# Optimization experiments

Hardware: AMD Instinct MI355X
Metric: run time of the kernel (lower is better)

## Reference

```python
import jax, jax.numpy as jnp
import numpy as np

N, E, F_IN, HID, HEADS, OUT, G = 50000, 800000, 128, 64, 4, 10, 64
NEG_SLOPE = 0.2


def _glorot(key, shape):
    fan = shape[0] + shape[-1]
    lim = np.sqrt(6.0 / fan)
    return jax.random.uniform(key, shape, jnp.float32, -lim, lim)


def setup_inputs() -> dict:
    key = jax.random.key(0)
    ks = jax.random.split(key, 20)
    x = jax.random.normal(ks[0], (N, F_IN), jnp.float32)
    edge_index = jax.random.randint(ks[1], (2, E), 0, N, jnp.int64)
    batch = jnp.sort(jax.random.randint(ks[2], (N,), 0, G, jnp.int64))
    inp = {"x": x, "edge_index": edge_index, "batch": batch}
    # layer 1: in=F_IN, heads=HEADS, out=HID
    inp["W1"] = _glorot(ks[3], (F_IN, HEADS * HID))
    inp["b1"] = jnp.zeros((HEADS * HID,), jnp.float32)
    inp["as1"] = _glorot(ks[4], (HEADS, HID))
    inp["ad1"] = _glorot(ks[5], (HEADS, HID))
    # layer 2: in=HEADS*HID, heads=HEADS, out=HID
    inp["W2"] = _glorot(ks[6], (HEADS * HID, HEADS * HID))
    inp["b2"] = jnp.zeros((HEADS * HID,), jnp.float32)
    inp["as2"] = _glorot(ks[7], (HEADS, HID))
    inp["ad2"] = _glorot(ks[8], (HEADS, HID))
    # layer 3: in=HEADS*HID, heads=1, out=HID
    inp["W3"] = _glorot(ks[9], (HEADS * HID, HID))
    inp["b3"] = jnp.zeros((HID,), jnp.float32)
    inp["as3"] = _glorot(ks[10], (1, HID))
    inp["ad3"] = _glorot(ks[11], (1, HID))
    # MLP head [HID, HID, OUT]
    inp["Wm1"] = _glorot(ks[12], (HID, HID))
    inp["bm1"] = jnp.zeros((HID,), jnp.float32)
    inp["Wm2"] = _glorot(ks[13], (HID, OUT))
    inp["bm2"] = jnp.zeros((OUT,), jnp.float32)
    return inp


def _gat_layer(x, src, dst, W, b, att_src, att_dst):
    # x: [N, Fin]; att_*: [H, C]
    H, C = att_src.shape
    h = (x @ W).reshape(N, H, C)
    a_src = jnp.einsum("nhc,hc->nh", h, att_src)
    a_dst = jnp.einsum("nhc,hc->nh", h, att_dst)
    alpha = jax.nn.leaky_relu(a_src[src] + a_dst[dst], NEG_SLOPE)  # [E', H]
    amax = jax.ops.segment_max(alpha, dst, num_segments=N)
    alpha = jnp.exp(alpha - amax[dst])
    denom = jax.ops.segment_sum(alpha, dst, num_segments=N)
    alpha = alpha / (denom[dst] + 1e-16)
    msg = h[src] * alpha[:, :, None]  # [E', H, C]
    out = jax.ops.segment_sum(msg, dst, num_segments=N)  # [N, H, C]
    return out.reshape(N, H * C) + b


def reference(x, edge_index, batch, W1, b1, as1, ad1, W2, b2, as2, ad2, W3, b3, as3, ad3, Wm1, bm1, Wm2, bm2):
    # PyG GATConv adds self-loops by default
    loops = jnp.arange(N, dtype=edge_index.dtype)
    src = jnp.concatenate([edge_index[0], loops])
    dst = jnp.concatenate([edge_index[1], loops])
    h = jax.nn.relu(_gat_layer(x, src, dst, W1, b1, as1, ad1))
    h = jax.nn.relu(_gat_layer(h, src, dst, W2, b2, as2, ad2))
    h = jax.nn.relu(_gat_layer(h, src, dst, W3, b3, as3, ad3))
    pooled = jax.ops.segment_sum(h, batch, num_segments=G)  # [G, HID]
    hidden = jax.nn.relu(pooled @ Wm1 + bm1)
    return hidden @ Wm2 + bm2
```

## Files before the change

kernel.cpp:

```cpp
#include <hip/hip_runtime.h>
#include <hip/hip_bf16.h>

#define F_IN   128
#define HID    64
#define HEADS  4
#define OUTD   10
#define NGRP   64

typedef unsigned short u16;
typedef __attribute__((ext_vector_type(8))) short short8;
typedef __attribute__((ext_vector_type(4))) float f32x4;

__device__ __forceinline__ float atomAddF(float* p, float v) {
    return __hip_atomic_fetch_add(p, v, __ATOMIC_RELAXED, __HIP_MEMORY_SCOPE_AGENT);
}
__device__ __forceinline__ float lrelu(float f) { return f > 0.f ? f : 0.2f * f; }
__device__ __forceinline__ float b2f(u16 u) { return __uint_as_float(((unsigned)u) << 16); }
__device__ __forceinline__ u16 f2b(float f) {
    unsigned u = __float_as_uint(f);
    return (u16)((u + 0x7fffu + ((u >> 16) & 1u)) >> 16);
}
__device__ __forceinline__ unsigned fmono(float f) {
    unsigned u = __float_as_uint(f);
    return (u & 0x80000000u) ? ~u : (u | 0x80000000u);
}
__device__ __forceinline__ float funmono(unsigned u) {
    return __uint_as_float((u & 0x80000000u) ? (u & 0x7FFFFFFFu) : ~u);
}

__global__ __launch_bounds__(256) void wtrans_all_kernel(const float* __restrict__ W1,
                                                         const float* __restrict__ W2,
                                                         const float* __restrict__ W3,
                                                         u16* __restrict__ Wt1,
                                                         u16* __restrict__ Wt2,
                                                         u16* __restrict__ Wt3) {
    int i = blockIdx.x * 256 + threadIdx.x;
    if (i < 32768) {
        int n = i >> 7, k = i & 127;
        Wt1[i] = f2b(W1[(size_t)k * 256 + n]);
    } else if (i < 98304) {
        int j = i - 32768;
        int n = j >> 8, k = j & 255;
        Wt2[j] = f2b(W2[(size_t)k * 256 + n]);
    } else if (i < 114688) {
        int j = i - 98304;
        int n = j >> 8, k = j & 255;
        Wt3[j] = f2b(W3[(size_t)k * 64 + n]);
    }
}

template<int K, int NC, bool AF32>
__global__ __launch_bounds__(256) void gemm_att_kernel(const void* __restrict__ Aptr,
                                                       const u16* __restrict__ Bt,
                                                       const float* __restrict__ as_,
                                                       const float* __restrict__ ad_,
                                                       u16* __restrict__ Hb,
                                                       float* __restrict__ a_src,
                                                       float* __restrict__ a_dst,
                                                       unsigned* __restrict__ gmaxu,
                                                       int nrows) {
    constexpr int LDA = 40;
    constexpr int HH = NC / 64;
    __shared__ u16 As[64][LDA];
    __shared__ u16 Bs[NC][LDA];
    int tid = threadIdx.x;
    int m0 = blockIdx.x * 64;
    int w = tid >> 6, l = tid & 63, lr = l & 15, lk = l >> 4;

    if constexpr (NC == 256) {
        f32x4 acc[4][4] = {};
        for (int k0 = 0; k0 < K; k0 += 32) {
            {
                int row = tid >> 2, ks = (tid & 3) * 8;
                int grow = m0 + row;
                short8 av = {};
                if (grow < nrows) {
                    if constexpr (AF32) {
                        const float* src = (const float*)Aptr + (size_t)grow * K + k0 + ks;
                        float4 v0 = *(const float4*)src;
                        float4 v1 = *(const float4*)(src + 4);
                        av[0] = (short)f2b(v0.x); av[1] = (short)f2b(v0.y);
                        av[2] = (short)f2b(v0.z); av[3] = (short)f2b(v0.w);
                        av[4] = (short)f2b(v1.x); av[5] = (short)f2b(v1.y);
                        av[6] = (short)f2b(v1.z); av[7] = (short)f2b(v1.w);
                    } else {
                        av = *(const short8*)&((const u16*)Aptr)[(size_t)grow * K + k0 + ks];
                    }
                }
                *(short8*)&As[row][ks] = av;
            }
            #pragma unroll
            for (int i = 0; i < 4; i++) {
                int col = (tid >> 2) + 64 * i;
                int ks = (tid & 3) * 8;
                *(short8*)&Bs[col][ks] = *(const short8*)&Bt[(size_t)col * K + k0 + ks];
            }
            __syncthreads();
            short8 a[4], b[4];
            #pragma unroll
            for (int mi = 0; mi < 4; mi++) a[mi] = *(const short8*)&As[16 * mi + lr][lk * 8];
            #pragma unroll
            for (int ni = 0; ni < 4; ni++) b[ni] = *(const short8*)&Bs[64 * w + 16 * ni + lr][lk * 8];
            #pragma unroll
            for (int mi = 0; mi < 4; mi++)
                #pragma unroll
                for (int ni = 0; ni < 4; ni++)
                    acc[mi][ni] = __builtin_amdgcn_mfma_f32_16x16x32_bf16(a[mi], b[ni], acc[mi][ni], 0, 0, 0);
            __syncthreads();
        }
        #pragma unroll
        for (int mi = 0; mi < 4; mi++) {
            #pragma unroll
            for (int j = 0; j < 4; j++) {
                int grow = m0 + 16 * mi + lk * 4 + j;
                if (grow < nrows) {
                    #pragma unroll
                    for (int ni = 0; ni < 4; ni++)
                        Hb[(size_t)grow * NC + 64 * w + 16 * ni + lr] = f2b(acc[mi][ni][j]);
                }
            }
        }
        float asv[4], adv[4];
        #pragma unroll
        for (int ni = 0; ni < 4; ni++) {
            asv[ni] = as_[w * 64 + 16 * ni + lr];
            adv[ni] = ad_[w * 64 + 16 * ni + lr];
        }
        float mxs = -3.4e38f;
        #pragma unroll
        for (int mi = 0; mi < 4; mi++) {
            #pragma unroll
            for (int j = 0; j < 4; j++) {
                float ps = 0.f, pd = 0.f;
                #pragma unroll
                for (int ni = 0; ni < 4; ni++) {
                    float v = acc[mi][ni][j];
                    ps += v * asv[ni];
                    pd += v * adv[ni];
                }
                #pragma unroll
                for (int o = 1; o < 16; o <<= 1) {
                    ps += __shfl_xor(ps, o, 64);
                    pd += __shfl_xor(pd, o, 64);
                }
                mxs = fmaxf(mxs, ps);
                int grow = m0 + 16 * mi + lk * 4 + j;
                if (lr == 0 && grow < nrows) {
                    a_src[grow * HH + w] = ps;
                    a_dst[grow * HH + w] = pd;
                }
            }
        }
        mxs = fmaxf(mxs, __shfl_xor(mxs, 16, 64));
        mxs = fmaxf(mxs, __shfl_xor(mxs, 32, 64));
        if (l == 0) atomicMax(&gmaxu[w], fmono(mxs));
    } else {
        f32x4 acc[4] = {};
        for (int k0 = 0; k0 < K; k0 += 32) {
            {
                int row = tid >> 2, ks = (tid & 3) * 8;
                int grow = m0 + row;
                short8 av = {};
                if (grow < nrows) av = *(const short8*)&((const u16*)Aptr)[(size_t)grow * K + k0 + ks];
                *(short8*)&As[row][ks] = av;
            }
            {
                int col = tid >> 2;
                int ks = (tid & 3) * 8;
                *(short8*)&Bs[col][ks] = *(const short8*)&Bt[(size_t)col * K + k0 + ks];
            }
            __syncthreads();
            short8 af = *(const short8*)&As[16 * w + lr][lk * 8];
            #pragma unroll
            for (int c = 0; c < 4; c++) {
                short8 bf = *(const short8*)&Bs[c * 16 + lr][lk * 8];
                acc[c] = __builtin_amdgcn_mfma_f32_16x16x32_bf16(af, bf, acc[c], 0, 0, 0);
            }
            __syncthreads();
        }
        #pragma unroll
        for (int c = 0; c < 4; c++) {
            #pragma unroll
            for (int j = 0; j < 4; j++) {
                int grow = m0 + 16 * w + lk * 4 + j;
                if (grow < nrows) Hb[(size_t)grow * NC + c * 16 + lr] = f2b(acc[c][j]);
            }
        }
        float asv[4], adv[4];
        #pragma unroll
        for (int c = 0; c < 4; c++) {
            asv[c] = as_[c * 16 + lr];
            adv[c] = ad_[c * 16 + lr];
        }
        float mxs = -3.4e38f;
        #pragma unroll
        for (int j = 0; j < 4; j++) {
            float ps = 0.f, pd = 0.f;
            #pragma unroll
            for (int c = 0; c < 4; c++) {
                float v = acc[c][j];
                ps += v * asv[c];
                pd += v * adv[c];
            }
            #pragma unroll
            for (int o = 1; o < 16; o <<= 1) {
                ps += __shfl_xor(ps, o, 64);
                pd += __shfl_xor(pd, o, 64);
            }
            mxs = fmaxf(mxs, ps);
            int grow = m0 + 16 * w + lk * 4 + j;
            if (lr == 0 && grow < nrows) {
                a_src[grow] = ps;
                a_dst[grow] = pd;
            }
        }
        mxs = fmaxf(mxs, __shfl_xor(mxs, 16, 64));
        mxs = fmaxf(mxs, __shfl_xor(mxs, 32, 64));
        if (l == 0) atomicMax(&gmaxu[0], fmono(mxs));
    }
}

__global__ void count_kernel(const int* __restrict__ ei, int* __restrict__ deg,
                             int E_, int n_nodes) {
    int e = blockIdx.x * 256 + threadIdx.x;
    int tot = E_ + n_nodes;
    if (e >= tot) return;
    int d = (e < E_) ? ei[E_ + e] : e - E_;
    atomicAdd(&deg[d], 1);
}

__global__ __launch_bounds__(256) void scan_reduce_kernel(const int* __restrict__ deg,
                                                          int* __restrict__ bsum, int n) {
    int i = blockIdx.x * 256 + threadIdx.x;
    int v = (i < n) ? deg[i] : 0;
    #pragma unroll
    for (int o = 32; o; o >>= 1) v += __shfl_xor(v, o, 64);
    __shared__ int ws[4];
    if ((threadIdx.x & 63) == 0) ws[threadIdx.x >> 6] = v;
    __syncthreads();
    if (threadIdx.x == 0) bsum[blockIdx.x] = ws[0] + ws[1] + ws[2] + ws[3];
}

__global__ __launch_bounds__(256) void scan_blocksums_kernel(int* __restrict__ bsum, int nb) {
    __shared__ int s[256];
    int t = threadIdx.x;
    int v = (t < nb) ? bsum[t] : 0;
    s[t] = v;
    __syncthreads();
    #pragma unroll
    for (int d = 1; d < 256; d <<= 1) {
        int x = (t >= d) ? s[t - d] : 0;
        __syncthreads();
        s[t] += x;
        __syncthreads();
    }
    if (t < nb) bsum[t] = s[t] - v;
}

__global__ __launch_bounds__(256) void scan_final_kernel(const int* __restrict__ deg,
                                                         const int* __restrict__ bsum,
                                                         int* __restrict__ off, int n) {
    __shared__ int s[256];
    int t = threadIdx.x;
    int i = blockIdx.x * 256 + t;
    int v = (i < n) ? deg[i] : 0;
    s[t] = v;
    __syncthreads();
    #pragma unroll
    for (int d = 1; d < 256; d <<= 1) {
        int x = (t >= d) ? s[t - d] : 0;
        __syncthreads();
        s[t] += x;
        __syncthreads();
    }
    int ex = s[t] - v + bsum[blockIdx.x];
    if (i < n) off[i] = ex;
    if (i == n - 1) off[n] = ex + v;
}

__global__ void fill_kernel(const int* __restrict__ ei, const int* __restrict__ off,
                            int* __restrict__ cursor, int* __restrict__ csr_src,
                            int E_, int n_nodes) {
    int e = blockIdx.x * 256 + threadIdx.x;
    int tot = E_ + n_nodes;
    if (e >= tot) return;
    int s, d;
    if (e < E_) { s = ei[e]; d = ei[E_ + e]; } else { s = d = e - E_; }
    int pos = atomicAdd(&cursor[d], 1);
    csr_src[off[d] + pos] = s;
}

template<int HH, int CPL, bool OUTF32>
__global__ __launch_bounds__(256) void gat_aggr_kernel(const int* __restrict__ off,
                                                       const int* __restrict__ csr_src,
                                                       const u16* __restrict__ Hb,
                                                       const float* __restrict__ a_src,
                                                       const float* __restrict__ a_dst,
                                                       const unsigned* __restrict__ gmaxu,
                                                       const float* __restrict__ bias,
                                                       u16* __restrict__ outb16,
                                                       float* __restrict__ outf32,
                                                       int n_nodes) {
    constexpr int HC = 64 * CPL;
    constexpr int GRP = 64 / HH;
    int d = blockIdx.x * 4 + (threadIdx.x >> 6);
    if (d >= n_nodes) return;
    int lane = threadIdx.x & 63;
    int hh = lane / GRP;
    int g = lane & (GRP - 1);
    int gb = lane & (64 - GRP);
    int o0 = off[d];
    int deg = off[d + 1] - o0;
    float adm = a_dst[d * HH + hh];
    float m = lrelu(funmono(gmaxu[hh]) + adm);

    float den = 0.f;
    float acc[CPL] = {};
    int j = 0;
    for (; j + 4 <= deg; j += 4) {
        int s0 = csr_src[o0 + j + 0];
        int s1 = csr_src[o0 + j + 1];
        int s2 = csr_src[o0 + j + 2];
        int s3 = csr_src[o0 + j + 3];
        int ssel = s3;
        if (g == 0) ssel = s0; else if (g == 1) ssel = s1; else if (g == 2) ssel = s2;
        float e = __expf(lrelu(a_src[ssel * HH + hh] + adm) - m);
        float e0 = __shfl(e, gb + 0, 64);
        float e1 = __shfl(e, gb + 1, 64);
        float e2 = __shfl(e, gb + 2, 64);
        float e3 = __shfl(e, gb + 3, 64);
        den += (e0 + e1) + (e2 + e3);
        if constexpr (CPL == 4) {
            uint2 h0 = *(const uint2*)&Hb[(size_t)s0 * HC + lane * 4];
            uint2 h1 = *(const uint2*)&Hb[(size_t)s1 * HC + lane * 4];
            uint2 h2 = *(const uint2*)&Hb[(size_t)s2 * HC + lane * 4];
            uint2 h3 = *(const uint2*)&Hb[(size_t)s3 * HC + lane * 4];
            acc[0] += e0 * __uint_as_float(h0.x << 16) + e1 * __uint_as_float(h1.x << 16)
                    + e2 * __uint_as_float(h2.x << 16) + e3 * __uint_as_float(h3.x << 16);
            acc[1] += e0 * __uint_as_float(h0.x & 0xffff0000u) + e1 * __uint_as_float(h1.x & 0xffff0000u)
                    + e2 * __uint_as_float(h2.x & 0xffff0000u) + e3 * __uint_as_float(h3.x & 0xffff0000u);
            acc[2] += e0 * __uint_as_float(h0.y << 16) + e1 * __uint_as_float(h1.y << 16)
                    + e2 * __uint_as_float(h2.y << 16) + e3 * __uint_as_float(h3.y << 16);
            acc[3] += e0 * __uint_as_float(h0.y & 0xffff0000u) + e1 * __uint_as_float(h1.y & 0xffff0000u)
                    + e2 * __uint_as_float(h2.y & 0xffff0000u) + e3 * __uint_as_float(h3.y & 0xffff0000u);
        } else {
            u16 h0 = Hb[(size_t)s0 * HC + lane];
            u16 h1 = Hb[(size_t)s1 * HC + lane];
            u16 h2 = Hb[(size_t)s2 * HC + lane];
            u16 h3 = Hb[(size_t)s3 * HC + lane];
            acc[0] += e0 * b2f(h0) + e1 * b2f(h1) + e2 * b2f(h2) + e3 * b2f(h3);
        }
    }
    for (; j < deg; j++) {
        int s = csr_src[o0 + j];
        float al = __expf(lrelu(a_src[s * HH + hh] + adm) - m);
        den += al;
        if constexpr (CPL == 4) {
            uint2 hv = *(const uint2*)&Hb[(size_t)s * HC + lane * 4];
            acc[0] += al * __uint_as_float(hv.x << 16);
            acc[1] += al * __uint_as_float(hv.x & 0xffff0000u);
            acc[2] += al * __uint_as_float(hv.y << 16);
            acc[3] += al * __uint_as_float(hv.y & 0xffff0000u);
        } else {
            acc[0] += al * b2f(Hb[(size_t)s * HC + lane]);
        }
    }
    float inv = 1.f / (den + 1e-16f);
    if constexpr (CPL == 4) {
        float4 bv = *(const float4*)&bias[lane * 4];
        float v0 = fmaxf(acc[0] * inv + bv.x, 0.f);
        float v1 = fmaxf(acc[1] * inv + bv.y, 0.f);
        float v2 = fmaxf(acc[2] * inv + bv.z, 0.f);
        float v3 = fmaxf(acc[3] * inv + bv.w, 0.f);
        uint2 o;
        o.x = (unsigned)f2b(v0) | ((unsigned)f2b(v1) << 16);
        o.y = (unsigned)f2b(v2) | ((unsigned)f2b(v3) << 16);
        *(uint2*)&outb16[(size_t)d * HC + lane * 4] = o;
    } else {
        float v = fmaxf(acc[0] * inv + bias[lane], 0.f);
        if constexpr (OUTF32) outf32[(size_t)d * HC + lane] = v;
        else                  outb16[(size_t)d * HC + lane] = f2b(v);
    }
}

__global__ __launch_bounds__(256) void pool_kernel(const float* __restrict__ H3,
                                                   const int* __restrict__ batch,
                                                   float* __restrict__ pooled, int n_nodes) {
    int wave = (blockIdx.x * 256 + threadIdx.x) >> 6;
    int lane = threadIdx.x & 63;
    int nwaves = gridDim.x * 4;
    int chunk = (n_nodes + nwaves - 1) / nwaves;
    int start = wave * chunk;
    int end = min(n_nodes, start + chunk);
    if (start >= end) return;
    int cur = batch[start];
    float acc = 0.f;
    for (int n = start; n < end; n++) {
        int g = batch[n];
        if (g != cur) { atomAddF(&pooled[cur * 64 + lane], acc); acc = 0.f; cur = g; }
        acc += H3[(size_t)n * 64 + lane];
    }
    atomAddF(&pooled[cur * 64 + lane], acc);
}

__global__ __launch_bounds__(64) void mlp_kernel(const float* __restrict__ pooled,
                                                 const float* __restrict__ Wm1,
                                                 const float* __restrict__ bm1,
                                                 const float* __restrict__ Wm2,
                                                 const float* __restrict__ bm2,
                                                 float* __restrict__ out) {
    __shared__ float sp[64], sh[64];
    int g = blockIdx.x, t = threadIdx.x;
    sp[t] = pooled[g * 64 + t];
    __syncthreads();
    float a = bm1[t];
    for (int k = 0; k < 64; k++) a += sp[k] * Wm1[k * 64 + t];
    sh[t] = a > 0.f ? a : 0.f;
    __syncthreads();
    if (t < 10) {
        float o = bm2[t];
        for (int j = 0; j < 64; j++) o += sh[j] * Wm2[j * 10 + t];
        out[g * 10 + t] = o;
    }
}

extern "C" void kernel_launch(void* const* d_in, const int* in_sizes, int n_in,
                              void* d_out, int out_size, void* d_ws, size_t ws_size,
                              hipStream_t stream) {
    const float* x   = (const float*)d_in[0];
    const int*   ei  = (const int*)d_in[1];
    const int*   bat = (const int*)d_in[2];
    const float* W1  = (const float*)d_in[3];
    const float* b1  = (const float*)d_in[4];
    const float* as1 = (const float*)d_in[5];
    const float* ad1 = (const float*)d_in[6];
    const float* W2  = (const float*)d_in[7];
    const float* b2  = (const float*)d_in[8];
    const float* as2 = (const float*)d_in[9];
    const float* ad2 = (const float*)d_in[10];
    const float* W3  = (const float*)d_in[11];
    const float* b3  = (const float*)d_in[12];
    const float* as3 = (const float*)d_in[13];
    const float* ad3 = (const float*)d_in[14];
    const float* Wm1 = (const float*)d_in[15];
    const float* bm1 = (const float*)d_in[16];
    const float* Wm2 = (const float*)d_in[17];
    const float* bm2 = (const float*)d_in[18];
    float* out = (float*)d_out;

    const int Nn = in_sizes[0] / F_IN;
    const int Ee = in_sizes[1] / 2;
    const int Et = Ee + Nn;

    char* wsp = (char*)d_ws;
    size_t off_b = 0;
    auto alloc = [&](size_t bytes) { void* p = wsp + off_b; off_b += (bytes + 255) & ~(size_t)255; return p; };
    u16*   HbA     = (u16*)alloc((size_t)Nn * 256 * 2);
    u16*   HbB     = (u16*)alloc((size_t)Nn * 256 * 2);
    float* Hf      = (float*)alloc((size_t)Nn * HID * 4);
    u16*   Wt1     = (u16*)alloc((size_t)256 * 128 * 2);
    u16*   Wt2     = (u16*)alloc((size_t)256 * 256 * 2);
    u16*   Wt3     = (u16*)alloc((size_t)64 * 256 * 2);
    float* a_src   = (float*)alloc((size_t)Nn * HEADS * 4);
    float* a_dst   = (float*)alloc((size_t)Nn * HEADS * 4);
    size_t zcount = 16 + (size_t)Nn * 2 + NGRP * HID;
    unsigned* zbase = (unsigned*)alloc(zcount * 4);
    unsigned* gmaxu = zbase;
    int*   deg     = (int*)(zbase + 16);
    int*   cursor  = deg + Nn;
    float* pooled  = (float*)(cursor + Nn);
    int*   bsum    = (int*)alloc((size_t)256 * 4);
    int*   csr_off = (int*)alloc((size_t)(Nn + 1) * 4);
    int*   csr_src = (int*)alloc((size_t)Et * 4);
    (void)ws_size;

    wtrans_all_kernel<<<(114688 + 255) / 256, 256, 0, stream>>>(W1, W2, W3, Wt1, Wt2, Wt3);

    hipMemsetAsync(zbase, 0, zcount * 4, stream);

    int eb = (Et + 255) / 256;
    int nb = (Nn + 255) / 256;
    count_kernel<<<eb, 256, 0, stream>>>(ei, deg, Ee, Nn);
    scan_reduce_kernel<<<nb, 256, 0, stream>>>(deg, bsum, Nn);
    scan_blocksums_kernel<<<1, 256, 0, stream>>>(bsum, nb);
    scan_final_kernel<<<nb, 256, 0, stream>>>(deg, bsum, csr_off, Nn);
    fill_kernel<<<eb, 256, 0, stream>>>(ei, csr_off, cursor, csr_src, Ee, Nn);

    const int gemm_blocks = (Nn + 63) / 64;
    const int nodeBlocks = (Nn + 3) / 4;

    gemm_att_kernel<128, 256, true><<<gemm_blocks, 256, 0, stream>>>(x, Wt1, as1, ad1,
                                                                     HbA, a_src, a_dst,
                                                                     gmaxu + 0, Nn);
    gat_aggr_kernel<4, 4, false><<<nodeBlocks, 256, 0, stream>>>(csr_off, csr_src, HbA,
                                                                 a_src, a_dst, gmaxu + 0, b1,
                                                                 HbB, nullptr, Nn);
    gemm_att_kernel<256, 256, false><<<gemm_blocks, 256, 0, stream>>>(HbB, Wt2, as2, ad2,
                                                                      HbA, a_src, a_dst,
                                                                      gmaxu + 4, Nn);
    gat_aggr_kernel<4, 4, false><<<nodeBlocks, 256, 0, stream>>>(csr_off, csr_src, HbA,
                                                                 a_src, a_dst, gmaxu + 4, b2,
                                                                 HbB, nullptr, Nn);
    gemm_att_kernel<256, 64, false><<<gemm_blocks, 256, 0, stream>>>(HbB, Wt3, as3, ad3,
                                                                     HbA, a_src, a_dst,
                                                                     gmaxu + 8, Nn);
    gat_aggr_kernel<1, 1, true><<<nodeBlocks, 256, 0, stream>>>(csr_off, csr_src, HbA,
                                                                a_src, a_dst, gmaxu + 8, b3,
                                                                nullptr, Hf, Nn);

    hipMemsetAsync(pooled, 0, (size_t)NGRP * HID * 4, stream);
    pool_kernel<<<128, 256, 0, stream>>>(Hf, bat, pooled, Nn);
    mlp_kernel<<<NGRP, 64, 0, stream>>>(pooled, Wm1, bm1, Wm2, bm2, out);
}
```

Baseline: 463.1 us.

## Enlarge GEMM row tile to 128 and split global max into separate kernel

The attention-projection GEMM now uses 512-thread blocks covering 128 rows, with an 8-wave layout of two row groups by four column groups, so each B tile is loaded once for twice as many rows. The per-block atomicMax of the source attention score is moved out of the GEMM into a small grid-stride gmax_kernel launched after each GEMM. The redundant memset of the pooled buffer is also dropped. This trims B-tile traffic and the GEMM epilogue, but adds three extra kernel launches and an extra read of a_src per layer.

```diff
diff --git a/kernel.cpp b/kernel.cpp
--- a/kernel.cpp
+++ b/kernel.cpp
@@ -50,24 +50,24 @@
 }
 
 template<int K, int NC, bool AF32>
-__global__ __launch_bounds__(256) void gemm_att_kernel(const void* __restrict__ Aptr,
+__global__ __launch_bounds__(512) void gemm_att_kernel(const void* __restrict__ Aptr,
                                                        const u16* __restrict__ Bt,
                                                        const float* __restrict__ as_,
                                                        const float* __restrict__ ad_,
                                                        u16* __restrict__ Hb,
                                                        float* __restrict__ a_src,
                                                        float* __restrict__ a_dst,
-                                                       unsigned* __restrict__ gmaxu,
                                                        int nrows) {
     constexpr int LDA = 40;
     constexpr int HH = NC / 64;
-    __shared__ u16 As[64][LDA];
+    __shared__ u16 As[128][LDA];
     __shared__ u16 Bs[NC][LDA];
     int tid = threadIdx.x;
-    int m0 = blockIdx.x * 64;
+    int m0 = blockIdx.x * 128;
     int w = tid >> 6, l = tid & 63, lr = l & 15, lk = l >> 4;
 
     if constexpr (NC == 256) {
+        int wr = w >> 2, wc = w & 3;
         f32x4 acc[4][4] = {};
         for (int k0 = 0; k0 < K; k0 += 32) {
             {
@@ -90,17 +90,17 @@
                 *(short8*)&As[row][ks] = av;
             }
             #pragma unroll
-            for (int i = 0; i < 4; i++) {
-                int col = (tid >> 2) + 64 * i;
+            for (int i = 0; i < 2; i++) {
+                int col = (tid >> 2) + 128 * i;
                 int ks = (tid & 3) * 8;
                 *(short8*)&Bs[col][ks] = *(const short8*)&Bt[(size_t)col * K + k0 + ks];
             }
             __syncthreads();
             short8 a[4], b[4];
             #pragma unroll
-            for (int mi = 0; mi < 4; mi++) a[mi] = *(const short8*)&As[16 * mi + lr][lk * 8];
-            #pragma unroll
-            for (int ni = 0; ni < 4; ni++) b[ni] = *(const short8*)&Bs[64 * w + 16 * ni + lr][lk * 8];
+            for (int mi = 0; mi < 4; mi++) a[mi] = *(const short8*)&As[64 * wr + 16 * mi + lr][lk * 8];
+            #pragma unroll
+            for (int ni = 0; ni < 4; ni++) b[ni] = *(const short8*)&Bs[64 * wc + 16 * ni + lr][lk * 8];
             #pragma unroll
             for (int mi = 0; mi < 4; mi++)
                 #pragma unroll
@@ -112,21 +112,20 @@
         for (int mi = 0; mi < 4; mi++) {
             #pragma unroll
             for (int j = 0; j < 4; j++) {
-                int grow = m0 + 16 * mi + lk * 4 + j;
+                int grow = m0 + 64 * wr + 16 * mi + lk * 4 + j;
                 if (grow < nrows) {
                     #pragma unroll
                     for (int ni = 0; ni < 4; ni++)
-                        Hb[(size_t)grow * NC + 64 * w + 16 * ni + lr] = f2b(acc[mi][ni][j]);
+                        Hb[(size_t)grow * NC + 64 * wc + 16 * ni + lr] = f2b(acc[mi][ni][j]);
                 }
             }
         }
         float asv[4], adv[4];
         #pragma unroll
         for (int ni = 0; ni < 4; ni++) {
-            asv[ni] = as_[w * 64 + 16 * ni + lr];
-            adv[ni] = ad_[w * 64 + 16 * ni + lr];
-        }
-        float mxs = -3.4e38f;
+            asv[ni] = as_[wc * 64 + 16 * ni + lr];
+            adv[ni] = ad_[wc * 64 + 16 * ni + lr];
+        }
         #pragma unroll
         for (int mi = 0; mi < 4; mi++) {
             #pragma unroll
@@ -143,17 +142,13 @@
                     ps += __shfl_xor(ps, o, 64);
                     pd += __shfl_xor(pd, o, 64);
                 }
-                mxs = fmaxf(mxs, ps);
-                int grow = m0 + 16 * mi + lk * 4 + j;
+                int grow = m0 + 64 * wr + 16 * mi + lk * 4 + j;
                 if (lr == 0 && grow < nrows) {
-                    a_src[grow * HH + w] = ps;
-                    a_dst[grow * HH + w] = pd;
+                    a_src[grow * HH + wc] = ps;
+                    a_dst[grow * HH + wc] = pd;
                 }
             }
         }
-        mxs = fmaxf(mxs, __shfl_xor(mxs, 16, 64));
-        mxs = fmaxf(mxs, __shfl_xor(mxs, 32, 64));
-        if (l == 0) atomicMax(&gmaxu[w], fmono(mxs));
     } else {
         f32x4 acc[4] = {};
         for (int k0 = 0; k0 < K; k0 += 32) {
@@ -164,7 +159,7 @@
                 if (grow < nrows) av = *(const short8*)&((const u16*)Aptr)[(size_t)grow * K + k0 + ks];
                 *(short8*)&As[row][ks] = av;
             }
-            {
+            if (tid < 256) {
                 int col = tid >> 2;
                 int ks = (tid & 3) * 8;
                 *(short8*)&Bs[col][ks] = *(const short8*)&Bt[(size_t)col * K + k0 + ks];
@@ -192,7 +187,6 @@
             asv[c] = as_[c * 16 + lr];
             adv[c] = ad_[c * 16 + lr];
         }
-        float mxs = -3.4e38f;
         #pragma unroll
         for (int j = 0; j < 4; j++) {
             float ps = 0.f, pd = 0.f;
@@ -207,16 +201,33 @@
                 ps += __shfl_xor(ps, o, 64);
                 pd += __shfl_xor(pd, o, 64);
             }
-            mxs = fmaxf(mxs, ps);
             int grow = m0 + 16 * w + lk * 4 + j;
             if (lr == 0 && grow < nrows) {
                 a_src[grow] = ps;
                 a_dst[grow] = pd;
             }
         }
-        mxs = fmaxf(mxs, __shfl_xor(mxs, 16, 64));
-        mxs = fmaxf(mxs, __shfl_xor(mxs, 32, 64));
-        if (l == 0) atomicMax(&gmaxu[0], fmono(mxs));
+    }
+}
+
+template<int HH>
+__global__ __launch_bounds__(256) void gmax_kernel(const float* __restrict__ a_src,
+                                                   unsigned* __restrict__ gmaxu, int n_nodes) {
+    float mx[HH];
+    #pragma unroll
+    for (int h = 0; h < HH; h++) mx[h] = -3.4e38f;
+    for (int i = blockIdx.x * 256 + threadIdx.x; i < n_nodes; i += gridDim.x * 256) {
+        #pragma unroll
+        for (int h = 0; h < HH; h++) mx[h] = fmaxf(mx[h], a_src[i * HH + h]);
+    }
+    #pragma unroll
+    for (int h = 0; h < HH; h++) {
+        #pragma unroll
+        for (int off = 32; off; off >>= 1) mx[h] = fmaxf(mx[h], __shfl_xor(mx[h], off, 64));
+    }
+    if ((threadIdx.x & 63) == 0) {
+        #pragma unroll
+        for (int h = 0; h < HH; h++) atomicMax(&gmaxu[h], fmono(mx[h]));
     }
 }
 
@@ -486,29 +497,28 @@
     scan_final_kernel<<<nb, 256, 0, stream>>>(deg, bsum, csr_off, Nn);
     fill_kernel<<<eb, 256, 0, stream>>>(ei, csr_off, cursor, csr_src, Ee, Nn);
 
-    const int gemm_blocks = (Nn + 63) / 64;
+    const int gemm_blocks = (Nn + 127) / 128;
     const int nodeBlocks = (Nn + 3) / 4;
 
-    gemm_att_kernel<128, 256, true><<<gemm_blocks, 256, 0, stream>>>(x, Wt1, as1, ad1,
-                                                                     HbA, a_src, a_dst,
-                                                                     gmaxu + 0, Nn);
+    gemm_att_kernel<128, 256, true><<<gemm_blocks, 512, 0, stream>>>(x, Wt1, as1, ad1,
+                                                                     HbA, a_src, a_dst, Nn);
+    gmax_kernel<4><<<64, 256, 0, stream>>>(a_src, gmaxu + 0, Nn);
     gat_aggr_kernel<4, 4, false><<<nodeBlocks, 256, 0, stream>>>(csr_off, csr_src, HbA,
                                                                  a_src, a_dst, gmaxu + 0, b1,
                                                                  HbB, nullptr, Nn);
-    gemm_att_kernel<256, 256, false><<<gemm_blocks, 256, 0, stream>>>(HbB, Wt2, as2, ad2,
-                                                                      HbA, a_src, a_dst,
-                                                                      gmaxu + 4, Nn);
+    gemm_att_kernel<256, 256, false><<<gemm_blocks, 512, 0, stream>>>(HbB, Wt2, as2, ad2,
+                                                                      HbA, a_src, a_dst, Nn);
+    gmax_kernel<4><<<64, 256, 0, stream>>>(a_src, gmaxu + 4, Nn);
     gat_aggr_kernel<4, 4, false><<<nodeBlocks, 256, 0, stream>>>(csr_off, csr_src, HbA,
                                                                  a_src, a_dst, gmaxu + 4, b2,
                                                                  HbB, nullptr, Nn);
-    gemm_att_kernel<256, 64, false><<<gemm_blocks, 256, 0, stream>>>(HbB, Wt3, as3, ad3,
-                                                                     HbA, a_src, a_dst,
-                                                                     gmaxu + 8, Nn);
+    gemm_att_kernel<256, 64, false><<<gemm_blocks, 512, 0, stream>>>(HbB, Wt3, as3, ad3,
+                                                                     HbA, a_src, a_dst, Nn);
+    gmax_kernel<1><<<64, 256, 0, stream>>>(a_src, gmaxu + 8, Nn);
     gat_aggr_kernel<1, 1, true><<<nodeBlocks, 256, 0, stream>>>(csr_off, csr_src, HbA,
                                                                 a_src, a_dst, gmaxu + 8, b3,
                                                                 nullptr, Hf, Nn);
 
-    hipMemsetAsync(pooled, 0, (size_t)NGRP * HID * 4, stream);
     pool_kernel<<<128, 256, 0, stream>>>(Hf, bat, pooled, Nn);
     mlp_kernel<<<NGRP, 64, 0, stream>>>(pooled, Wm1, bm1, Wm2, bm2, out);
 }
```

Result: faster. 402.0 us (-13.2%).
